# Performance work log

Measured on AMD Instinct MI355X. Metric: run time of the kernel, lower is better.

## Reference

```python
import jax, jax.numpy as jnp
import numpy as np

IGNORE_INDEX = -100


def setup_inputs() -> dict:
    key = jax.random.key(0)
    k1, k2 = jax.random.split(key)
    logits = jax.random.normal(k1, (8, 19, 512, 512), dtype=jnp.float32)
    labels = jax.random.randint(k2, (8, 512, 512), 0, 19, dtype=jnp.int64)
    return {"logits": logits, "labels": labels}


def reference(logits, labels):
    # Lovasz-Softmax loss (CoinCheung/pytorch-loss LovaszSoftmaxV3, reduction='mean').
    n, c, h, w = logits.shape
    lg = jnp.moveaxis(logits, 1, 0).reshape(c, -1).astype(jnp.float32)  # [C, P]
    lb = labels.reshape(-1)  # [P]
    valid = (lb != IGNORE_INDEX)

    probs = jax.nn.softmax(lg, axis=0)  # [C, P]
    # one-hot labels, zeroed at ignored pixels
    onehot = ((jnp.arange(c)[:, None] == lb[None, :]) & valid[None, :]).astype(jnp.float32)

    errs = jnp.abs(onehot - probs)
    # push ignored pixels to the end of the descending sort with sentinel -1
    errs = jnp.where(valid[None, :], errs, jnp.float32(-1.0))

    order = jnp.argsort(-errs, axis=1)  # descending sort per class
    errs_sort = jnp.take_along_axis(errs, order, axis=1)
    oh_sort = jnp.take_along_axis(onehot, order, axis=1)

    # Lovasz extension gradient (jacc), computed without autodiff flow
    n_pos = oh_sort.sum(axis=1, keepdims=True)
    inter = n_pos - jnp.cumsum(oh_sort, axis=1)
    union = n_pos + jnp.cumsum(1.0 - oh_sort, axis=1)
    jacc = 1.0 - inter / union
    jacc = jnp.concatenate([jacc[:, :1], jacc[:, 1:] - jacc[:, :-1]], axis=1)

    # ignored pixels have errs_sort = -1 -> relu zeroes their contribution
    losses = jnp.sum(jax.nn.relu(errs_sort) * jacc, axis=1)  # per-class [C]
    return losses.mean()
```

## Files before the change

### kernel.cpp

```cpp
#include <hip/hip_runtime.h>
#include <hip/hip_bf16.h>

#define NCLASS 19
#define BINS 512
#define NB (NCLASS * BINS)
#define NREP 4
#define RPAD 8
#define RSTRIDE (NB + RPAD)
#define SLICES 8
#define IGNORE_IDX (-100)
#define HW_SHIFT 18
#define HW_C (1 << HW_SHIFT)

#define LOADSET(V, LB, PIX)                                                  \
  {                                                                          \
    int n_ = (PIX) >> HW_SHIFT;                                              \
    int hw_ = (PIX) & (HW_C - 1);                                            \
    const float* lp_ =                                                       \
        logits + (((size_t)n_ * NCLASS) << HW_SHIFT) + hw_;                  \
    _Pragma("unroll") for (int c_ = 0; c_ < NCLASS; ++c_) {                  \
      float2 q_ = *(const float2*)(lp_ + ((size_t)c_ << HW_SHIFT));          \
      V[c_][0] = q_.x;                                                       \
      V[c_][1] = q_.y;                                                       \
    }                                                                        \
    LB = *(const int2*)(labels + (PIX));                                     \
  }

#define PROCSET(V, LB)                                                       \
  {                                                                          \
    float m0_ = -3.4e38f, m1_ = -3.4e38f;                                    \
    _Pragma("unroll") for (int c_ = 0; c_ < NCLASS; ++c_) {                  \
      m0_ = fmaxf(m0_, V[c_][0]);                                            \
      m1_ = fmaxf(m1_, V[c_][1]);                                            \
    }                                                                        \
    float s0_ = 0.f, s1_ = 0.f;                                              \
    _Pragma("unroll") for (int c_ = 0; c_ < NCLASS; ++c_) {                  \
      V[c_][0] = __expf(V[c_][0] - m0_); s0_ += V[c_][0];                    \
      V[c_][1] = __expf(V[c_][1] - m1_); s1_ += V[c_][1];                    \
    }                                                                        \
    float i0_ = 1.0f / s0_, i1_ = 1.0f / s1_;                                \
    int l0_ = LB.x, l1_ = LB.y;                                              \
    _Pragma("unroll") for (int c_ = 0; c_ < NCLASS; ++c_) {                  \
      if (l0_ != IGNORE_IDX) {                                               \
        float pr_ = V[c_][0] * i0_;                                          \
        bool pos_ = (c_ == l0_);                                             \
        float e_ = pos_ ? (1.0f - pr_) : pr_;                                \
        int b_ = min(BINS - 1, (int)(e_ * (float)BINS));                     \
        atomicAdd(&sh[rep + (c_ << 9) + b_], pos_ ? 0x10000u : 1u);          \
      }                                                                      \
      if (l1_ != IGNORE_IDX) {                                               \
        float pr_ = V[c_][1] * i1_;                                          \
        bool pos_ = (c_ == l1_);                                             \
        float e_ = pos_ ? (1.0f - pr_) : pr_;                                \
        int b_ = min(BINS - 1, (int)(e_ * (float)BINS));                     \
        atomicAdd(&sh[rep + (c_ << 9) + b_], pos_ ? 0x10000u : 1u);          \
      }                                                                      \
    }                                                                        \
  }

__global__ void __launch_bounds__(1024, 4) hist_pf(
    const float* __restrict__ logits, const int* __restrict__ labels,
    unsigned* __restrict__ copies, int P, int ppb) {
  extern __shared__ unsigned sh[];
  for (int i = threadIdx.x; i < NREP * RSTRIDE; i += 1024) sh[i] = 0u;
  __syncthreads();

  const int rep = (threadIdx.x & 3) * RSTRIDE;
  const int STEP = 1024 * 2;
  int p1 = min(P, blockIdx.x * ppb + ppb);
  int p = blockIdx.x * ppb + (int)threadIdx.x * 2;

  float va[NCLASS][2], vb[NCLASS][2];
  int2 la, lb;
  bool has = p < p1;
  if (has) LOADSET(va, la, p);
  while (has) {
    int pn = p + STEP;
    bool hasn = pn < p1;
    if (hasn) LOADSET(vb, lb, pn);
    PROCSET(va, la);
    p = pn;
    has = hasn;
    if (!has) break;
    pn = p + STEP;
    hasn = pn < p1;
    if (hasn) LOADSET(va, la, pn);
    PROCSET(vb, lb);
    p = pn;
    has = hasn;
  }
  __syncthreads();

  unsigned* dst = copies + (size_t)blockIdx.x * NB;
  for (int i = threadIdx.x; i < NB; i += 1024)
    dst[i] =
        sh[i] + sh[RSTRIDE + i] + sh[2 * RSTRIDE + i] + sh[3 * RSTRIDE + i];
}

__global__ void __launch_bounds__(256) reduce_part(
    const unsigned* __restrict__ copies, unsigned long long* __restrict__ part,
    int R) {
  const int nblk = NB / 256;
  int s = blockIdx.x / nblk;
  int blk = blockIdx.x - s * nblk;
  int cb = blk * 256 + threadIdx.x;
  unsigned long long acc = 0;
  for (int r = s; r < R; r += SLICES) {
    unsigned v = copies[(size_t)r * NB + cb];
    acc += ((unsigned long long)(v >> 16) << 32) |
           (unsigned long long)(v & 0xffffu);
  }
  part[(size_t)s * NB + cb] = acc;
}

__global__ void __launch_bounds__(256) scan19_fold(
    const unsigned long long* __restrict__ part, float* __restrict__ partial) {
  int c = blockIdx.x;
  __shared__ unsigned long long bins[BINS];
  __shared__ unsigned long long arr[256];
  __shared__ unsigned long long wsum[4];
  __shared__ float fsum[4];
  int tid = threadIdx.x;

  for (int i = tid; i < BINS; i += 256) {
    unsigned long long a = 0;
#pragma unroll
    for (int s = 0; s < SLICES; ++s) a += part[(size_t)s * NB + c * BINS + i];
    bins[i] = a;
  }
  __syncthreads();

  unsigned long long t = 0;
  for (int i = tid; i < BINS; i += 256) t += bins[i];
  for (int off = 32; off > 0; off >>= 1) t += __shfl_down(t, off, 64);
  int lane = tid & 63, w = tid >> 6;
  if (lane == 0) wsum[w] = t;
  __syncthreads();
  unsigned long long total = wsum[0] + wsum[1] + wsum[2] + wsum[3];
  float nPos = (float)(unsigned)(total >> 32);

  unsigned long long above = 0;
  float acc = 0.f;
  for (int r = BINS / 256 - 1; r >= 0; --r) {
    arr[tid] = bins[r * 256 + tid];
    __syncthreads();
    for (int off = 1; off < 256; off <<= 1) {
      unsigned long long add = (tid + off < 256) ? arr[tid + off] : 0ull;
      __syncthreads();
      arr[tid] += add;
      __syncthreads();
    }
    unsigned long long suff = arr[tid] + above;
    unsigned long long rowTot = arr[0];
    __syncthreads();

    int gb = r * 256 + tid;
    if (gb >= 1) {
      float CP = (float)(unsigned)(suff >> 32);
      float CN = (float)(unsigned)(suff & 0xffffffffull);
      float uni = nPos + CN;
      if (uni > 0.f) acc += 1.0f - (nPos - CP) / uni;
    }
    above += rowTot;
  }

  for (int off = 32; off > 0; off >>= 1) acc += __shfl_down(acc, off, 64);
  if (lane == 0) fsum[w] = acc;
  __syncthreads();
  if (tid == 0) partial[c] = fsum[0] + fsum[1] + fsum[2] + fsum[3];
}

__global__ void __launch_bounds__(64) lovasz_final(
    const float* __restrict__ partial, float* __restrict__ out, int n,
    float scale) {
  float acc = 0.f;
  for (int i = threadIdx.x; i < n; i += 64) acc += partial[i];
  for (int off = 32; off > 0; off >>= 1) acc += __shfl_down(acc, off, 64);
  if (threadIdx.x == 0) out[0] = acc * scale;
}

extern "C" void kernel_launch(void* const* d_in, const int* in_sizes, int n_in,
                              void* d_out, int out_size, void* d_ws,
                              size_t ws_size, hipStream_t stream) {
  const float* logits = (const float*)d_in[0];
  const int* labels = (const int*)d_in[1];
  float* out = (float*)d_out;

  const int P = in_sizes[1];

  int R = 256;
  while (R > 32 &&
         (size_t)R * NB * 4 + (size_t)SLICES * NB * 8 + 4096 > ws_size)
    R >>= 1;
  int ppb = ((P + R - 1) / R + 2047) & ~2047;

  char* ws = (char*)d_ws;
  unsigned* copies = (unsigned*)ws;
  unsigned long long* part = (unsigned long long*)(ws + (size_t)R * NB * 4);
  float* partial = (float*)(part + (size_t)SLICES * NB);

  size_t ldsBytes = (size_t)NREP * RSTRIDE * 4;

  hist_pf<<<R, 1024, ldsBytes, stream>>>(logits, labels, copies, P, ppb);
  reduce_part<<<SLICES * (NB / 256), 256, 0, stream>>>(copies, part, R);
  scan19_fold<<<NCLASS, 256, 0, stream>>>(part, partial);
  lovasz_final<<<1, 64, 0, stream>>>(partial, out, NCLASS,
                                     1.0f / ((float)BINS * (float)NCLASS));
}
```

Before: 52.97 us.

## Fuse reduction, per-class scan and final mean into one kernel via atomic tickets

Merges the partial reduction, per-class scan and final averaging kernels into a single launch. The last 19 blocks to finish, identified by an atomic ticket counter, each spin-wait until every block has written its partial sums, then scan one class, and the last class block computes the mean. The reduction loop is also unrolled by four with independent accumulators. This removes two kernel launches and their gaps, at the cost of a memset launch, spin-waiting, and an assumption that the ticket-based waiting never deadlocks.

```diff
diff --git a/kernel.cpp b/kernel.cpp
--- a/kernel.cpp
+++ b/kernel.cpp
@@ -8,9 +8,14 @@
 #define RPAD 8
 #define RSTRIDE (NB + RPAD)
 #define SLICES 8
+#define NGRID (SLICES * (NB / 256))
 #define IGNORE_IDX (-100)
 #define HW_SHIFT 18
 #define HW_C (1 << HW_SHIFT)
+
+#define UNPACK(v)                                            \
+  (((unsigned long long)((v) >> 16) << 32) |                 \
+   (unsigned long long)((v) & 0xffffu))
 
 #define LOADSET(V, LB, PIX)                                                  \
   {                                                                          \
@@ -97,35 +102,56 @@
         sh[i] + sh[RSTRIDE + i] + sh[2 * RSTRIDE + i] + sh[3 * RSTRIDE + i];
 }
 
-__global__ void __launch_bounds__(256) reduce_part(
+__global__ void __launch_bounds__(256) tail_fused(
     const unsigned* __restrict__ copies, unsigned long long* __restrict__ part,
-    int R) {
+    float* __restrict__ partial, unsigned* __restrict__ counters,
+    float* __restrict__ out, int R) {
   const int nblk = NB / 256;
   int s = blockIdx.x / nblk;
   int blk = blockIdx.x - s * nblk;
   int cb = blk * 256 + threadIdx.x;
-  unsigned long long acc = 0;
-  for (int r = s; r < R; r += SLICES) {
-    unsigned v = copies[(size_t)r * NB + cb];
-    acc += ((unsigned long long)(v >> 16) << 32) |
-           (unsigned long long)(v & 0xffffu);
-  }
-  part[(size_t)s * NB + cb] = acc;
-}
-
-__global__ void __launch_bounds__(256) scan19_fold(
-    const unsigned long long* __restrict__ part, float* __restrict__ partial) {
-  int c = blockIdx.x;
+  int tid = threadIdx.x;
+
+  unsigned long long a0 = 0, a1 = 0, a2 = 0, a3 = 0;
+  for (int r = s; r < R; r += 4 * SLICES) {
+    unsigned v0 = copies[(size_t)r * NB + cb];
+    unsigned v1 = copies[(size_t)(r + SLICES) * NB + cb];
+    unsigned v2 = copies[(size_t)(r + 2 * SLICES) * NB + cb];
+    unsigned v3 = copies[(size_t)(r + 3 * SLICES) * NB + cb];
+    a0 += UNPACK(v0);
+    a1 += UNPACK(v1);
+    a2 += UNPACK(v2);
+    a3 += UNPACK(v3);
+  }
+  part[(size_t)s * NB + cb] = (a0 + a1) + (a2 + a3);
+
+  __shared__ unsigned tk;
+  __threadfence();
+  __syncthreads();
+  if (tid == 0) tk = atomicAdd(&counters[0], 1u);
+  __syncthreads();
+  unsigned ticket = tk;
+  if (ticket < NGRID - NCLASS) return;
+  int c = (int)ticket - (NGRID - NCLASS);
+
+  if (tid == 0) {
+    while (__hip_atomic_load(&counters[0], __ATOMIC_ACQUIRE,
+                             __HIP_MEMORY_SCOPE_AGENT) < NGRID) {
+    }
+  }
+  __syncthreads();
+  __threadfence();
+
   __shared__ unsigned long long bins[BINS];
   __shared__ unsigned long long arr[256];
   __shared__ unsigned long long wsum[4];
   __shared__ float fsum[4];
-  int tid = threadIdx.x;
 
   for (int i = tid; i < BINS; i += 256) {
     unsigned long long a = 0;
 #pragma unroll
-    for (int s = 0; s < SLICES; ++s) a += part[(size_t)s * NB + c * BINS + i];
+    for (int sl = 0; sl < SLICES; ++sl)
+      a += part[(size_t)sl * NB + (c << 9) + i];
     bins[i] = a;
   }
   __syncthreads();
@@ -167,16 +193,19 @@
   for (int off = 32; off > 0; off >>= 1) acc += __shfl_down(acc, off, 64);
   if (lane == 0) fsum[w] = acc;
   __syncthreads();
-  if (tid == 0) partial[c] = fsum[0] + fsum[1] + fsum[2] + fsum[3];
-}
-
-__global__ void __launch_bounds__(64) lovasz_final(
-    const float* __restrict__ partial, float* __restrict__ out, int n,
-    float scale) {
-  float acc = 0.f;
-  for (int i = threadIdx.x; i < n; i += 64) acc += partial[i];
-  for (int off = 32; off > 0; off >>= 1) acc += __shfl_down(acc, off, 64);
-  if (threadIdx.x == 0) out[0] = acc * scale;
+
+  if (tid == 0) {
+    partial[c] = fsum[0] + fsum[1] + fsum[2] + fsum[3];
+    __threadfence();
+    unsigned t2 = atomicAdd(&counters[1], 1u);
+    if (t2 == NCLASS - 1) {
+      __threadfence();
+      float m = 0.f;
+#pragma unroll
+      for (int i = 0; i < NCLASS; ++i) m += partial[i];
+      out[0] = m * (1.0f / ((float)BINS * (float)NCLASS));
+    }
+  }
 }
 
 extern "C" void kernel_launch(void* const* d_in, const int* in_sizes, int n_in,
@@ -198,12 +227,13 @@
   unsigned* copies = (unsigned*)ws;
   unsigned long long* part = (unsigned long long*)(ws + (size_t)R * NB * 4);
   float* partial = (float*)(part + (size_t)SLICES * NB);
+  unsigned* counters = (unsigned*)(partial + 32);
 
   size_t ldsBytes = (size_t)NREP * RSTRIDE * 4;
 
+  hipMemsetAsync(counters, 0, 2 * sizeof(unsigned), stream);
+
   hist_pf<<<R, 1024, ldsBytes, stream>>>(logits, labels, copies, P, ppb);
-  reduce_part<<<SLICES * (NB / 256), 256, 0, stream>>>(copies, part, R);
-  scan19_fold<<<NCLASS, 256, 0, stream>>>(part, partial);
-  lovasz_final<<<1, 64, 0, stream>>>(partial, out, NCLASS,
-                                     1.0f / ((float)BINS * (float)NCLASS));
+  tail_fused<<<NGRID, 256, 0, stream>>>(copies, part, partial, counters, out,
+                                        R);
 }
```

Measured after the change: 76.45 us. 1.44x slower.
